# Kernel tuning notes

Measured on AMD Instinct MI355X. Metric: run time of the kernel, lower is better.

## Reference

```python
import jax, jax.numpy as jnp
import numpy as np

H, D, DM, L, B = 16, 64, 1024, 256, 64
SCALE = 1.0 / np.sqrt(D)   # 1/sqrt(d_head)
CHUNK = 64
LN_EPS = 1e-5


def setup_inputs() -> dict:
    key = jax.random.key(0)
    k0, k1, k2, k3 = jax.random.split(key, 4)
    h = jax.random.normal(k0, (L, B, DM), jnp.float32)
    qkv_w = jax.random.normal(k1, (H * 4 * D, DM), jnp.float32) * 0.02
    o_w = jax.random.normal(k2, (DM, H * D), jnp.float32) * 0.02
    ln_gamma = jnp.ones((DM,), jnp.float32)
    ln_beta = jnp.zeros((DM,), jnp.float32)
    pi0 = jax.random.uniform(k3, (H, 256), jnp.float32)
    return {"h": h, "qkv_w": qkv_w, "o_w": o_w,
            "ln_gamma": ln_gamma, "ln_beta": ln_beta, "pi0": pi0}


def _phi(x):
    # elu(x) + 1, then sum-normalize over feature dim
    e = jax.nn.elu(x) + 1.0
    return e / e.sum(-1, keepdims=True)


def _fast_weight_sum(q, k, v):
    # q,k,v: [B,H,L,D]. out[t] = q_t @ W_t, W_t = sum_{s<=t} k_s v_s^T (inclusive).
    # Chunked-recurrent form: intra-chunk causal GEMM + inter-chunk carried state.
    Bb, Hh, Ll, Dd = q.shape
    nc = Ll // CHUNK
    rs = lambda x: x.reshape(Bb, Hh, nc, CHUNK, Dd).transpose(2, 0, 1, 3, 4)  # [nc,B,H,C,D]
    qc, kc, vc = rs(q), rs(k), rs(v)
    mask = jnp.tril(jnp.ones((CHUNK, CHUNK), q.dtype))  # inclusive causal

    def step(W, xs):
        qi, ki, vi = xs  # [B,H,C,D]
        scores = jnp.einsum('bhtd,bhsd->bhts', qi, ki) * mask
        out = jnp.einsum('bhts,bhsd->bhtd', scores, vi) \
            + jnp.einsum('bhtd,bhde->bhte', qi, W)
        W = W + jnp.einsum('bhsd,bhse->bhde', ki, vi)
        return W, out

    W0 = jnp.zeros((Bb, Hh, Dd, Dd), q.dtype)
    _, outs = jax.lax.scan(step, W0, (qc, kc, vc))  # outs: [nc,B,H,C,D]
    return outs.transpose(1, 2, 0, 3, 4).reshape(Bb, Hh, Ll, Dd)


def reference(h, qkv_w, o_w, ln_gamma, ln_beta, pi0):
    slen, bsz, _ = h.shape
    # qkv projection and head split (rbf2keys: q, k1, k2, v)
    qkv = (h @ qkv_w.T).reshape(slen, bsz, H, 4 * D)
    hq, hk1, hk2, hv = jnp.split(qkv, 4, axis=-1)       # each [L,B,H,D]
    perm = lambda x: x.transpose(1, 2, 0, 3)            # -> [B,H,L,D]
    hq, hk1, hk2, hv = perm(hq), perm(hk1), perm(hk2), perm(hv)

    hq = _phi(hq)
    hk1 = _phi(hk1)
    hk2 = _phi(hk2)

    out1 = _fast_weight_sum(hq, hk1, hv)
    out2 = _fast_weight_sum(hq, hk2, hv)

    # skip_attn_normalization=True path: pi0-gated mixture of the two memories
    p = jnp.clip(pi0, 0.0, 1.0)[None, :, :slen, None]   # [1,H,L,1]
    layer_out = SCALE * (out1 * p + out2 * (1.0 - p))   # [B,H,L,D]

    # [B,H,L,D] -> [L,B,H*D]
    layer_out = layer_out.transpose(0, 2, 1, 3).reshape(bsz, slen, H * D).transpose(1, 0, 2)
    attn_out = layer_out @ o_w.T                        # [L,B,DM]

    # post-LN residual (pre_lnorm=False)
    x = h + attn_out
    mu = x.mean(-1, keepdims=True)
    var = ((x - mu) ** 2).mean(-1, keepdims=True)
    return (x - mu) / jnp.sqrt(var + LN_EPS) * ln_gamma + ln_beta
```

## Files before the change

kernel.cpp:

```cpp
#include <hip/hip_runtime.h>
#include <type_traits>


typedef short v8s __attribute__((ext_vector_type(8)));
typedef float v4f __attribute__((ext_vector_type(4)));

__device__ __forceinline__ float bf2f(short s) {
    unsigned int u = ((unsigned int)(unsigned short)s) << 16;
    float f;
    __builtin_memcpy(&f, &u, 4);
    return f;
}
__device__ __forceinline__ short f2bf(float f) {
    unsigned int u;
    __builtin_memcpy(&u, &f, 4);
    u = u + 0x7fffu + ((u >> 16) & 1u);
    return (short)(u >> 16);
}

__device__ __forceinline__ void load_lds16(const short* g, short* l) {
    __builtin_amdgcn_global_load_lds((const __attribute__((address_space(1))) void*)g,
                                     (__attribute__((address_space(3))) void*)l, 16, 0, 0);
}

__global__ void __launch_bounds__(256)
cvt_bf16(const float* __restrict__ in, short* __restrict__ out, int n4) {
    int i = blockIdx.x * 256 + threadIdx.x;
    if (i >= n4) return;
    float4 v = ((const float4*)in)[i];
    short4 o;
    o.x = f2bf(v.x); o.y = f2bf(v.y); o.z = f2bf(v.z); o.w = f2bf(v.w);
    ((short4*)out)[i] = o;
}

template <typename OutT>
__global__ void __launch_bounds__(512, 2)
gemm_nt(const short* __restrict__ Ap, const short* __restrict__ Bp,
        OutT* __restrict__ C, int M, int N, int K) {
    __shared__ __align__(16) short lds[2][2][256 * 64];

    const int tid = threadIdx.x;
    const int w = tid >> 6, lane = tid & 63;
    const int wm = w >> 2, wn = w & 3;
    const int lq = lane >> 4, lr = lane & 15;
    const int asw = (lr & 7) * 8;
    const int rr = tid >> 3;
    const int scol = ((tid & 7) * 8) ^ ((rr & 7) * 8);

    int bid = blockIdx.y * gridDim.x + blockIdx.x;
    int bm, bn;
    if (gridDim.x == 64) {
        int xcd = bid & 7, u = bid >> 3;
        bm = xcd * 8 + (u & 7);
        bn = u >> 3;
    } else {
        int nwg = gridDim.x * gridDim.y;
        int swz = (bid & 7) * (nwg >> 3) + (bid >> 3);
        bm = swz % gridDim.x; bn = swz / gridDim.x;
    }

    v4f acc[8][4] = {};
    v8s a[4][2];
    v8s b[2][2][2];

    const int NT = K >> 6;
    const int nIter = NT >> 1;

#define BAR_() do { asm volatile("" ::: "memory"); __builtin_amdgcn_s_barrier(); asm volatile("" ::: "memory"); } while (0)
#define SBAR_() __builtin_amdgcn_sched_barrier(0)
#define VMCNT4_() asm volatile("s_waitcnt vmcnt(4)" ::: "memory")
#define STAGE_(MAT, BUF, HALF, KT) do { \
        const short* g_ = ((MAT) ? Bp : Ap) + \
            (long)(((MAT) ? bn : bm) * 256 + (HALF) * 128 + rr) * K + (KT) * 64 + scol; \
        short* l_ = &lds[BUF][MAT][(HALF) * 8192] + w * 512; \
        load_lds16(g_, l_); \
        load_lds16(g_ + (long)64 * K, l_ + 4096); \
    } while (0)
#define LDA_(QM, BUF) do { \
        _Pragma("unroll") \
        for (int mi = 0; mi < 4; ++mi) { \
            const short* pa_ = &lds[BUF][0][(wm * 128 + (QM) * 64 + mi * 16 + lr) * 64]; \
            a[mi][0] = *(const v8s*)&pa_[(lq * 8) ^ asw]; \
            a[mi][1] = *(const v8s*)&pa_[(32 + lq * 8) ^ asw]; \
        } \
    } while (0)
#define LDB_(QN, BUF) do { \
        _Pragma("unroll") \
        for (int ni = 0; ni < 2; ++ni) { \
            const short* pb_ = &lds[BUF][1][(wn * 64 + (QN) * 32 + ni * 16 + lr) * 64]; \
            b[QN][ni][0] = *(const v8s*)&pb_[(lq * 8) ^ asw]; \
            b[QN][ni][1] = *(const v8s*)&pb_[(32 + lq * 8) ^ asw]; \
        } \
    } while (0)
#define MFMA_(QM, QN) do { \
        __builtin_amdgcn_s_setprio(1); \
        _Pragma("unroll") \
        for (int kk = 0; kk < 2; ++kk) \
            _Pragma("unroll") \
            for (int mi = 0; mi < 4; ++mi) \
                _Pragma("unroll") \
                for (int ni = 0; ni < 2; ++ni) \
                    acc[(QM) * 4 + mi][(QN) * 2 + ni] = __builtin_amdgcn_mfma_f32_16x16x32_bf16( \
                        a[mi][kk], b[QN][ni][kk], acc[(QM) * 4 + mi][(QN) * 2 + ni], 0, 0, 0); \
        __builtin_amdgcn_s_setprio(0); \
    } while (0)

    STAGE_(1, 0, 0, 0);
    STAGE_(1, 0, 1, 0);
    STAGE_(0, 0, 0, 0);
    STAGE_(0, 0, 1, 0);
    STAGE_(1, 1, 0, 1);
    STAGE_(1, 1, 1, 1);
    VMCNT4_();
    BAR_();

    for (int it = 0; it < nIter; ++it) {
        const int t1 = 2 * it + 1;
        int t2 = 2 * it + 2; if (t2 >= NT) t2 -= NT;
        int t3 = 2 * it + 3; if (t3 >= NT) t3 -= NT;

        LDA_(0, 0); LDB_(0, 0); LDB_(1, 0);
        STAGE_(0, 1, 0, t1);
        MFMA_(0, 0);
        SBAR_(); BAR_();
        STAGE_(0, 1, 1, t1);
        MFMA_(0, 1);
        SBAR_();
        LDA_(1, 0);
        SBAR_(); BAR_();
        STAGE_(1, 0, 0, t2);
        MFMA_(1, 0);
        SBAR_(); BAR_();
        STAGE_(1, 0, 1, t2);
        VMCNT4_();
        MFMA_(1, 1);
        SBAR_(); BAR_();
        LDA_(0, 1); LDB_(0, 1); LDB_(1, 1);
        STAGE_(0, 0, 0, t2);
        MFMA_(0, 0);
        SBAR_(); BAR_();
        STAGE_(0, 0, 1, t2);
        MFMA_(0, 1);
        SBAR_();
        LDA_(1, 1);
        SBAR_(); BAR_();
        STAGE_(1, 1, 0, t3);
        MFMA_(1, 0);
        SBAR_(); BAR_();
        STAGE_(1, 1, 1, t3);
        VMCNT4_();
        MFMA_(1, 1);
        SBAR_(); BAR_();
    }

#undef BAR_
#undef SBAR_
#undef VMCNT4_
#undef STAGE_
#undef LDA_
#undef LDB_
#undef MFMA_

#pragma unroll
    for (int m = 0; m < 8; ++m)
#pragma unroll
        for (int n = 0; n < 4; ++n)
#pragma unroll
            for (int r = 0; r < 4; ++r) {
                int row = bm * 256 + wm * 128 + m * 16 + lq * 4 + r;
                int col = bn * 256 + wn * 64 + n * 16 + lr;
                float v = acc[m][n][r];
                if constexpr (std::is_same_v<OutT, short>)
                    C[(long)row * N + col] = f2bf(v);
                else
                    C[(long)row * N + col] = v;
            }
}

#define SZF(row, col) (((row) << 6) + ((col) ^ (((row) & 7) << 3)))
#define LGKM0_() do { asm volatile("s_waitcnt lgkmcnt(0)" ::: "memory"); __builtin_amdgcn_sched_barrier(0); } while (0)

__device__ __forceinline__ void phi_lane(short* area, int lane) {
    v8s r[8];
#pragma unroll
    for (int g = 0; g < 8; g++)
        r[g] = *(const v8s*)&area[SZF(lane, g * 8)];
    float s = 0.f;
#pragma unroll
    for (int g = 0; g < 8; g++)
#pragma unroll
        for (int k = 0; k < 8; k++) {
            float x = bf2f(r[g][k]);
            s += x > 0.f ? x + 1.f : __expf(x);
        }
    float inv = 1.f / s;
#pragma unroll
    for (int g = 0; g < 8; g++) {
        v8s o;
#pragma unroll
        for (int k = 0; k < 8; k++) {
            float x = bf2f(r[g][k]);
            float e = x > 0.f ? x + 1.f : __expf(x);
            o[k] = f2bf(e * inv);
        }
        *(v8s*)&area[SZF(lane, g * 8)] = o;
    }
}

__device__ __forceinline__ void transpose_lane(short* area, int lane) {
    v8s r[8];
#pragma unroll
    for (int g = 0; g < 8; g++)
        r[g] = *(const v8s*)&area[SZF(lane, g * 8)];
    LGKM0_();
#pragma unroll
    for (int g = 0; g < 8; g++)
#pragma unroll
        for (int k = 0; k < 8; k++)
            area[SZF(g * 8 + k, lane)] = r[g][k];
}

__global__ void __launch_bounds__(64)
fwA(const short* __restrict__ qkv, short* __restrict__ wpre) {
    const int bid = blockIdx.x;
    const int b = bid & 63, h = (bid >> 6) & 15, mem = bid >> 10;
    const int lane = threadIdx.x;
    const int lq = lane >> 4, lr = lane & 15;
    __shared__ __align__(16) short Ak[4096];
    __shared__ __align__(16) short Av[4096];

    const int srow = lane >> 3;
    const int scolw = ((lane & 7) ^ (srow & 7)) << 3;
    const int koff = 64 + mem * 64;

    v4f wacc[4][4] = {};

    for (int c = 0; c < 3; c++) {
        LGKM0_();
        {
            const short* g = qkv + ((long)((c * 64 + srow) * 64 + b)) * 4096 + h * 256 + koff + scolw;
#pragma unroll
            for (int i = 0; i < 8; i++)
                load_lds16(g + (long)i * 8 * 64 * 4096, Ak + i * 512);
        }
        {
            const short* g = qkv + ((long)((c * 64 + srow) * 64 + b)) * 4096 + h * 256 + 192 + scolw;
#pragma unroll
            for (int i = 0; i < 8; i++)
                load_lds16(g + (long)i * 8 * 64 * 4096, Av + i * 512);
        }
        asm volatile("s_waitcnt vmcnt(0)" ::: "memory");
        __builtin_amdgcn_sched_barrier(0);

        phi_lane(Ak, lane);
        transpose_lane(Av, lane);
        LGKM0_();

        v8s vf[4][2];
#pragma unroll
        for (int i = 0; i < 4; i++)
#pragma unroll
            for (int kk = 0; kk < 2; kk++)
                vf[i][kk] = *(const v8s*)&Av[SZF(16 * i + lr, 32 * kk + 8 * lq)];
#pragma unroll
        for (int n = 0; n < 4; n++) {
            v8s ktb[2];
#pragma unroll
            for (int kk = 0; kk < 2; kk++) {
                v8s t;
#pragma unroll
                for (int e = 0; e < 8; e++)
                    t[e] = Ak[SZF(32 * kk + 8 * lq + e, 16 * n + lr)];
                ktb[kk] = t;
            }
#pragma unroll
            for (int i = 0; i < 4; i++) {
                wacc[i][n] = __builtin_amdgcn_mfma_f32_16x16x32_bf16(vf[i][0], ktb[0], wacc[i][n], 0, 0, 0);
                wacc[i][n] = __builtin_amdgcn_mfma_f32_16x16x32_bf16(vf[i][1], ktb[1], wacc[i][n], 0, 0, 0);
            }
        }
        short* wp = wpre + (((long)(mem * 3 + c) * 16 + h) * 64 + b) * 4096;
#pragma unroll
        for (int i = 0; i < 4; i++)
#pragma unroll
            for (int n = 0; n < 4; n++)
#pragma unroll
                for (int r2 = 0; r2 < 4; r2++)
                    wp[(16 * i + lq * 4 + r2) * 64 + 16 * n + lr] = f2bf(wacc[i][n][r2]);
    }
}

__global__ void __launch_bounds__(256)
fwB(const short* __restrict__ qkv, const short* __restrict__ wpre,
    const float* __restrict__ pi0, short* __restrict__ outm) {
    const int bid = blockIdx.x;
    const int b = bid & 63, h = (bid >> 6) & 15, c = bid >> 10;
    const int tid = threadIdx.x;
    const int wv = tid >> 6, lane = tid & 63;
    const int lq = lane >> 4, lr = lane & 15;
    __shared__ __align__(16) short sq[4096];
    __shared__ __align__(16) short sk1[4096];
    __shared__ __align__(16) short sk2[4096];
    __shared__ __align__(16) short svT[4096];

    const int srow = lane >> 3;
    const int scolw = ((lane & 7) ^ (srow & 7)) << 3;

    {
        short* area = (wv == 0) ? sq : (wv == 1) ? sk1 : (wv == 2) ? sk2 : svT;
        const short* g = qkv + ((long)((c * 64 + srow) * 64 + b)) * 4096 + h * 256 + wv * 64 + scolw;
#pragma unroll
        for (int i = 0; i < 8; i++)
            load_lds16(g + (long)i * 8 * 64 * 4096, area + i * 512);
    }
    asm volatile("s_waitcnt vmcnt(0)" ::: "memory");
    __syncthreads();

    if (wv == 0)      phi_lane(sq, lane);
    else if (wv == 1) phi_lane(sk1, lane);
    else if (wv == 2) phi_lane(sk2, lane);
    else              transpose_lane(svT, lane);
    __syncthreads();

    v8s qa[2];
    qa[0] = *(const v8s*)&sq[SZF(16 * wv + lr, 8 * lq)];
    qa[1] = *(const v8s*)&sq[SZF(16 * wv + lr, 32 + 8 * lq)];

    v8s wb1[4][2], wb2[4][2];
    if (c > 0) {
        const short* w1 = wpre + (((long)(0 * 3 + (c - 1)) * 16 + h) * 64 + b) * 4096;
        const short* w2 = wpre + (((long)(1 * 3 + (c - 1)) * 16 + h) * 64 + b) * 4096;
#pragma unroll
        for (int n = 0; n < 4; n++)
#pragma unroll
            for (int kk = 0; kk < 2; kk++) {
                wb1[n][kk] = *(const v8s*)&w1[(16 * n + lr) * 64 + 32 * kk + 8 * lq];
                wb2[n][kk] = *(const v8s*)&w2[(16 * n + lr) * 64 + 32 * kk + 8 * lq];
            }
    }
    float pv[4];
#pragma unroll
    for (int r2 = 0; r2 < 4; r2++) {
        float p = pi0[h * 256 + c * 64 + 16 * wv + lq * 4 + r2];
        pv[r2] = fminf(fmaxf(p, 0.f), 1.f);
    }

    v4f sacc1[4], sacc2[4];
#pragma unroll
    for (int n = 0; n < 4; n++) {
        v8s b10 = *(const v8s*)&sk1[SZF(16 * n + lr, 8 * lq)];
        v8s b11 = *(const v8s*)&sk1[SZF(16 * n + lr, 32 + 8 * lq)];
        v8s b20 = *(const v8s*)&sk2[SZF(16 * n + lr, 8 * lq)];
        v8s b21 = *(const v8s*)&sk2[SZF(16 * n + lr, 32 + 8 * lq)];
        v4f t1 = {}, t2 = {};
        t1 = __builtin_amdgcn_mfma_f32_16x16x32_bf16(qa[0], b10, t1, 0, 0, 0);
        t2 = __builtin_amdgcn_mfma_f32_16x16x32_bf16(qa[0], b20, t2, 0, 0, 0);
        t1 = __builtin_amdgcn_mfma_f32_16x16x32_bf16(qa[1], b11, t1, 0, 0, 0);
        t2 = __builtin_amdgcn_mfma_f32_16x16x32_bf16(qa[1], b21, t2, 0, 0, 0);
        sacc1[n] = t1; sacc2[n] = t2;
    }
    __syncthreads();

#pragma unroll
    for (int n = 0; n < 4; n++)
#pragma unroll
        for (int r2 = 0; r2 < 4; r2++) {
            int t_ = 16 * wv + lq * 4 + r2;
            int s_ = 16 * n + lr;
            sk1[SZF(t_, s_)] = f2bf(s_ <= t_ ? sacc1[n][r2] : 0.f);
            sk2[SZF(t_, s_)] = f2bf(s_ <= t_ ? sacc2[n][r2] : 0.f);
        }
    LGKM0_();

    v8s sa1[2], sa2[2];
    sa1[0] = *(const v8s*)&sk1[SZF(16 * wv + lr, 8 * lq)];
    sa1[1] = *(const v8s*)&sk1[SZF(16 * wv + lr, 32 + 8 * lq)];
    sa2[0] = *(const v8s*)&sk2[SZF(16 * wv + lr, 8 * lq)];
    sa2[1] = *(const v8s*)&sk2[SZF(16 * wv + lr, 32 + 8 * lq)];

#pragma unroll
    for (int j = 0; j < 4; j++) {
        v8s vb0 = *(const v8s*)&svT[SZF(16 * j + lr, 8 * lq)];
        v8s vb1 = *(const v8s*)&svT[SZF(16 * j + lr, 32 + 8 * lq)];
        v4f t1 = {}, t2 = {};
        t1 = __builtin_amdgcn_mfma_f32_16x16x32_bf16(sa1[0], vb0, t1, 0, 0, 0);
        t2 = __builtin_amdgcn_mfma_f32_16x16x32_bf16(sa2[0], vb0, t2, 0, 0, 0);
        t1 = __builtin_amdgcn_mfma_f32_16x16x32_bf16(sa1[1], vb1, t1, 0, 0, 0);
        t2 = __builtin_amdgcn_mfma_f32_16x16x32_bf16(sa2[1], vb1, t2, 0, 0, 0);
        if (c > 0) {
            t1 = __builtin_amdgcn_mfma_f32_16x16x32_bf16(qa[0], wb1[j][0], t1, 0, 0, 0);
            t2 = __builtin_amdgcn_mfma_f32_16x16x32_bf16(qa[0], wb2[j][0], t2, 0, 0, 0);
            t1 = __builtin_amdgcn_mfma_f32_16x16x32_bf16(qa[1], wb1[j][1], t1, 0, 0, 0);
            t2 = __builtin_amdgcn_mfma_f32_16x16x32_bf16(qa[1], wb2[j][1], t2, 0, 0, 0);
        }
#pragma unroll
        for (int r2 = 0; r2 < 4; r2++) {
            int t_ = 16 * wv + lq * 4 + r2;
            float val = 0.125f * (pv[r2] * t1[r2] + (1.f - pv[r2]) * t2[r2]);
            outm[((long)((c * 64 + t_) * 64 + b)) * 1024 + h * 64 + 16 * j + lr] = f2bf(val);
        }
    }
}

__global__ void __launch_bounds__(256)
ln_kernel(const float* __restrict__ h, const float* __restrict__ attn,
          const float* __restrict__ gamma, const float* __restrict__ beta,
          float* __restrict__ out) {
    const int row = blockIdx.x;
    const long base = (long)row * 1024;
    const int tid = threadIdx.x;
    float4 xh = ((const float4*)(h + base))[tid];
    float4 xa = ((const float4*)(attn + base))[tid];
    float4 x;
    x.x = xh.x + xa.x; x.y = xh.y + xa.y; x.z = xh.z + xa.z; x.w = xh.w + xa.w;
    float s = x.x + x.y + x.z + x.w;
    float s2 = x.x * x.x + x.y * x.y + x.z * x.z + x.w * x.w;
#pragma unroll
    for (int m = 32; m > 0; m >>= 1) {
        s += __shfl_xor(s, m, 64);
        s2 += __shfl_xor(s2, m, 64);
    }
    __shared__ float ps[4], ps2[4];
    int w = tid >> 6, lane = tid & 63;
    if (lane == 0) { ps[w] = s; ps2[w] = s2; }
    __syncthreads();
    s = ps[0] + ps[1] + ps[2] + ps[3];
    s2 = ps2[0] + ps2[1] + ps2[2] + ps2[3];
    float mu = s * (1.f / 1024.f);
    float var = s2 * (1.f / 1024.f) - mu * mu;
    float inv = rsqrtf(var + 1e-5f);
    float4 g = ((const float4*)gamma)[tid];
    float4 bb = ((const float4*)beta)[tid];
    float4 o;
    o.x = (x.x - mu) * inv * g.x + bb.x;
    o.y = (x.y - mu) * inv * g.y + bb.y;
    o.z = (x.z - mu) * inv * g.z + bb.z;
    o.w = (x.w - mu) * inv * g.w + bb.w;
    ((float4*)(out + base))[tid] = o;
}

extern "C" void kernel_launch(void* const* d_in, const int* in_sizes, int n_in,
                              void* d_out, int out_size, void* d_ws, size_t ws_size,
                              hipStream_t stream) {
    const float* h     = (const float*)d_in[0];
    const float* qkvw  = (const float*)d_in[1];
    const float* ow    = (const float*)d_in[2];
    const float* gamma = (const float*)d_in[3];
    const float* beta  = (const float*)d_in[4];
    const float* pi0   = (const float*)d_in[5];
    float* out = (float*)d_out;
    char* ws = (char*)d_ws;

    short* h_bf   = (short*)(ws);
    short* wq_bf  = (short*)(ws + 33554432);
    short* wo_bf  = (short*)(ws + 41943040);
    short* qkv_bf = (short*)(ws + 44040192);
    short* wpre   = (short*)(ws + 178257920);
    float* attnf  = (float*)(ws + 44040192);
    short* lmix   = h_bf;

    cvt_bf16<<<16384, 256, 0, stream>>>(h, h_bf, 16777216 / 4);
    cvt_bf16<<<4096, 256, 0, stream>>>(qkvw, wq_bf, 4194304 / 4);
    cvt_bf16<<<1024, 256, 0, stream>>>(ow, wo_bf, 1048576 / 4);

    gemm_nt<short><<<dim3(64, 16), 512, 0, stream>>>(h_bf, wq_bf, qkv_bf, 16384, 4096, 1024);

    fwA<<<2048, 64, 0, stream>>>(qkv_bf, wpre);
    fwB<<<4096, 256, 0, stream>>>(qkv_bf, wpre, pi0, lmix);

    gemm_nt<float><<<dim3(64, 4), 512, 0, stream>>>(lmix, wo_bf, attnf, 16384, 1024, 1024);

    ln_kernel<<<16384, 256, 0, stream>>>(h, attnf, gamma, beta, out);
}
```

Measured before the change: 412.0 us.

## Shrink GEMM tiles to 256x128xK32, stage fwA stores and fwB weights via LDS

The GEMM is retiled from 256x256 with K-step 64 to 256x128 with K-step 32. This cuts LDS per block so four blocks can share a CU, and doubles the grid. The swizzle and pipeline schedule are rewritten to match, with a single B load per stage. Separately, fwA now stages its fast-weight output through LDS so it can write coalesced 16-byte rows, and fwB loads the carried state into LDS asynchronously instead of doing strided global reads. The smaller tiles lower per-block arithmetic intensity and add more barriers per unit of work, while fwB grows its shared-memory footprint.

```diff
diff --git a/kernel.cpp b/kernel.cpp
--- a/kernel.cpp
+++ b/kernel.cpp
@@ -34,84 +34,68 @@
 }
 
 template <typename OutT>
-__global__ void __launch_bounds__(512, 2)
+__global__ void __launch_bounds__(512, 4)
 gemm_nt(const short* __restrict__ Ap, const short* __restrict__ Bp,
         OutT* __restrict__ C, int M, int N, int K) {
-    __shared__ __align__(16) short lds[2][2][256 * 64];
+    __shared__ __align__(16) short ldsA[2][256 * 32];
+    __shared__ __align__(16) short ldsB[2][128 * 32];
 
     const int tid = threadIdx.x;
     const int w = tid >> 6, lane = tid & 63;
     const int wm = w >> 2, wn = w & 3;
     const int lq = lane >> 4, lr = lane & 15;
-    const int asw = (lr & 7) * 8;
-    const int rr = tid >> 3;
-    const int scol = ((tid & 7) * 8) ^ ((rr & 7) * 8);
+    const int asw = (lq ^ ((lr >> 1) & 3)) * 8;
+    const int rr = tid >> 2;
+    const int scol = ((tid & 3) ^ ((rr >> 1) & 3)) * 8;
 
     int bid = blockIdx.y * gridDim.x + blockIdx.x;
-    int bm, bn;
-    if (gridDim.x == 64) {
-        int xcd = bid & 7, u = bid >> 3;
-        bm = xcd * 8 + (u & 7);
-        bn = u >> 3;
-    } else {
-        int nwg = gridDim.x * gridDim.y;
-        int swz = (bid & 7) * (nwg >> 3) + (bid >> 3);
-        bm = swz % gridDim.x; bn = swz / gridDim.x;
-    }
-
-    v4f acc[8][4] = {};
-    v8s a[4][2];
-    v8s b[2][2][2];
-
-    const int NT = K >> 6;
+    int xcd = bid & 7, u = bid >> 3;
+    int bm = xcd * 8 + (u & 7);
+    int bn = u >> 3;
+
+    v4f acc[8][2] = {};
+    v8s a[4], b[2];
+
+    const int NT = K >> 5;
     const int nIter = NT >> 1;
+
+    const short* baseA0 = Ap + (long)(bm * 256 + rr) * K + scol;
+    const short* baseA1 = baseA0 + (long)128 * K;
+    const short* baseB  = Bp + (long)(bn * 128 + rr) * K + scol;
 
 #define BAR_() do { asm volatile("" ::: "memory"); __builtin_amdgcn_s_barrier(); asm volatile("" ::: "memory"); } while (0)
 #define SBAR_() __builtin_amdgcn_sched_barrier(0)
-#define VMCNT4_() asm volatile("s_waitcnt vmcnt(4)" ::: "memory")
-#define STAGE_(MAT, BUF, HALF, KT) do { \
-        const short* g_ = ((MAT) ? Bp : Ap) + \
-            (long)(((MAT) ? bn : bm) * 256 + (HALF) * 128 + rr) * K + (KT) * 64 + scol; \
-        short* l_ = &lds[BUF][MAT][(HALF) * 8192] + w * 512; \
-        load_lds16(g_, l_); \
-        load_lds16(g_ + (long)64 * K, l_ + 4096); \
+#define VMCNT1_() asm volatile("s_waitcnt vmcnt(1)" ::: "memory")
+#define STAGEA_(BUF, HALF, KT) \
+    load_lds16(((HALF) ? baseA1 : baseA0) + (KT) * 32, &ldsA[BUF][(HALF) * 4096 + w * 512])
+#define STAGEB_(BUF, KT) \
+    load_lds16(baseB + (KT) * 32, &ldsB[BUF][w * 512])
+#define LDA_(H, BUF) do { \
+        _Pragma("unroll") \
+        for (int mi = 0; mi < 4; ++mi) \
+            a[mi] = *(const v8s*)&ldsA[BUF][(wm * 128 + (H) * 64 + mi * 16 + lr) * 32 + asw]; \
     } while (0)
-#define LDA_(QM, BUF) do { \
+#define LDB_(BUF) do { \
         _Pragma("unroll") \
-        for (int mi = 0; mi < 4; ++mi) { \
-            const short* pa_ = &lds[BUF][0][(wm * 128 + (QM) * 64 + mi * 16 + lr) * 64]; \
-            a[mi][0] = *(const v8s*)&pa_[(lq * 8) ^ asw]; \
-            a[mi][1] = *(const v8s*)&pa_[(32 + lq * 8) ^ asw]; \
-        } \
+        for (int ni = 0; ni < 2; ++ni) \
+            b[ni] = *(const v8s*)&ldsB[BUF][(wn * 32 + ni * 16 + lr) * 32 + asw]; \
     } while (0)
-#define LDB_(QN, BUF) do { \
-        _Pragma("unroll") \
-        for (int ni = 0; ni < 2; ++ni) { \
-            const short* pb_ = &lds[BUF][1][(wn * 64 + (QN) * 32 + ni * 16 + lr) * 64]; \
-            b[QN][ni][0] = *(const v8s*)&pb_[(lq * 8) ^ asw]; \
-            b[QN][ni][1] = *(const v8s*)&pb_[(32 + lq * 8) ^ asw]; \
-        } \
-    } while (0)
-#define MFMA_(QM, QN) do { \
+#define MFMA_(H) do { \
         __builtin_amdgcn_s_setprio(1); \
         _Pragma("unroll") \
-        for (int kk = 0; kk < 2; ++kk) \
+        for (int mi = 0; mi < 4; ++mi) \
             _Pragma("unroll") \
-            for (int mi = 0; mi < 4; ++mi) \
-                _Pragma("unroll") \
-                for (int ni = 0; ni < 2; ++ni) \
-                    acc[(QM) * 4 + mi][(QN) * 2 + ni] = __builtin_amdgcn_mfma_f32_16x16x32_bf16( \
-                        a[mi][kk], b[QN][ni][kk], acc[(QM) * 4 + mi][(QN) * 2 + ni], 0, 0, 0); \
+            for (int ni = 0; ni < 2; ++ni) \
+                acc[(H) * 4 + mi][ni] = __builtin_amdgcn_mfma_f32_16x16x32_bf16( \
+                    a[mi], b[ni], acc[(H) * 4 + mi][ni], 0, 0, 0); \
         __builtin_amdgcn_s_setprio(0); \
     } while (0)
 
-    STAGE_(1, 0, 0, 0);
-    STAGE_(1, 0, 1, 0);
-    STAGE_(0, 0, 0, 0);
-    STAGE_(0, 0, 1, 0);
-    STAGE_(1, 1, 0, 1);
-    STAGE_(1, 1, 1, 1);
-    VMCNT4_();
+    STAGEB_(0, 0);
+    STAGEA_(0, 0, 0);
+    STAGEA_(0, 1, 0);
+    STAGEB_(1, 1);
+    VMCNT1_();
     BAR_();
 
     for (int it = 0; it < nIter; ++it) {
@@ -119,44 +103,37 @@
         int t2 = 2 * it + 2; if (t2 >= NT) t2 -= NT;
         int t3 = 2 * it + 3; if (t3 >= NT) t3 -= NT;
 
-        LDA_(0, 0); LDB_(0, 0); LDB_(1, 0);
-        STAGE_(0, 1, 0, t1);
-        MFMA_(0, 0);
-        SBAR_(); BAR_();
-        STAGE_(0, 1, 1, t1);
-        MFMA_(0, 1);
+        LDA_(0, 0); LDB_(0);
+        STAGEA_(1, 0, t1);
+        MFMA_(0);
         SBAR_();
         LDA_(1, 0);
         SBAR_(); BAR_();
-        STAGE_(1, 0, 0, t2);
-        MFMA_(1, 0);
-        SBAR_(); BAR_();
-        STAGE_(1, 0, 1, t2);
-        VMCNT4_();
-        MFMA_(1, 1);
-        SBAR_(); BAR_();
-        LDA_(0, 1); LDB_(0, 1); LDB_(1, 1);
-        STAGE_(0, 0, 0, t2);
-        MFMA_(0, 0);
-        SBAR_(); BAR_();
-        STAGE_(0, 0, 1, t2);
-        MFMA_(0, 1);
+        STAGEA_(1, 1, t1);
+        STAGEB_(0, t2);
+        MFMA_(1);
+        SBAR_();
+        VMCNT1_();
+        BAR_();
+        LDA_(0, 1); LDB_(1);
+        STAGEA_(0, 0, t2);
+        MFMA_(0);
         SBAR_();
         LDA_(1, 1);
         SBAR_(); BAR_();
-        STAGE_(1, 1, 0, t3);
-        MFMA_(1, 0);
-        SBAR_(); BAR_();
-        STAGE_(1, 1, 1, t3);
-        VMCNT4_();
-        MFMA_(1, 1);
-        SBAR_(); BAR_();
+        STAGEA_(0, 1, t2);
+        STAGEB_(1, t3);
+        MFMA_(1);
+        SBAR_();
+        VMCNT1_();
+        BAR_();
     }
 
 #undef BAR_
 #undef SBAR_
-#undef VMCNT4_
-#undef STAGE_
+#undef VMCNT1_
+#undef STAGEA_
+#undef STAGEB_
 #undef LDA_
 #undef LDB_
 #undef MFMA_
@@ -164,11 +141,11 @@
 #pragma unroll
     for (int m = 0; m < 8; ++m)
 #pragma unroll
-        for (int n = 0; n < 4; ++n)
+        for (int n = 0; n < 2; ++n)
 #pragma unroll
             for (int r = 0; r < 4; ++r) {
                 int row = bm * 256 + wm * 128 + m * 16 + lq * 4 + r;
-                int col = bn * 256 + wn * 64 + n * 16 + lr;
+                int col = bn * 128 + wn * 32 + n * 16 + lr;
                 float v = acc[m][n][r];
                 if constexpr (std::is_same_v<OutT, short>)
                     C[(long)row * N + col] = f2bf(v);
@@ -279,14 +256,21 @@
                 wacc[i][n] = __builtin_amdgcn_mfma_f32_16x16x32_bf16(vf[i][1], ktb[1], wacc[i][n], 0, 0, 0);
             }
         }
+        LGKM0_();
+#pragma unroll
+        for (int i = 0; i < 4; i++)
+#pragma unroll
+            for (int n = 0; n < 4; n++)
+#pragma unroll
+                for (int r2 = 0; r2 < 4; r2++)
+                    Av[SZF(16 * i + lq * 4 + r2, 16 * n + lr)] = f2bf(wacc[i][n][r2]);
+        LGKM0_();
         short* wp = wpre + (((long)(mem * 3 + c) * 16 + h) * 64 + b) * 4096;
 #pragma unroll
-        for (int i = 0; i < 4; i++)
-#pragma unroll
-            for (int n = 0; n < 4; n++)
-#pragma unroll
-                for (int r2 = 0; r2 < 4; r2++)
-                    wp[(16 * i + lq * 4 + r2) * 64 + 16 * n + lr] = f2bf(wacc[i][n][r2]);
+        for (int g = 0; g < 8; g++) {
+            v8s t = *(const v8s*)&Av[SZF(lane, g * 8)];
+            *(v8s*)(wp + lane * 64 + g * 8) = t;
+        }
     }
 }
 
@@ -302,6 +286,8 @@
     __shared__ __align__(16) short sk1[4096];
     __shared__ __align__(16) short sk2[4096];
     __shared__ __align__(16) short svT[4096];
+    __shared__ __align__(16) short sw1[4096];
+    __shared__ __align__(16) short sw2[4096];
 
     const int srow = lane >> 3;
     const int scolw = ((lane & 7) ^ (srow & 7)) << 3;
@@ -312,6 +298,14 @@
 #pragma unroll
         for (int i = 0; i < 8; i++)
             load_lds16(g + (long)i * 8 * 64 * 4096, area + i * 512);
+    }
+    if (c > 0 && wv < 2) {
+        short* area = wv ? sw2 : sw1;
+        const short* g = wpre + (((long)(wv * 3 + (c - 1)) * 16 + h) * 64 + b) * 4096
+                       + srow * 64 + scolw;
+#pragma unroll
+        for (int i = 0; i < 8; i++)
+            load_lds16(g + (long)i * 8 * 64, area + i * 512);
     }
     asm volatile("s_waitcnt vmcnt(0)" ::: "memory");
     __syncthreads();
@@ -328,14 +322,12 @@
 
     v8s wb1[4][2], wb2[4][2];
     if (c > 0) {
-        const short* w1 = wpre + (((long)(0 * 3 + (c - 1)) * 16 + h) * 64 + b) * 4096;
-        const short* w2 = wpre + (((long)(1 * 3 + (c - 1)) * 16 + h) * 64 + b) * 4096;
 #pragma unroll
         for (int n = 0; n < 4; n++)
 #pragma unroll
             for (int kk = 0; kk < 2; kk++) {
-                wb1[n][kk] = *(const v8s*)&w1[(16 * n + lr) * 64 + 32 * kk + 8 * lq];
-                wb2[n][kk] = *(const v8s*)&w2[(16 * n + lr) * 64 + 32 * kk + 8 * lq];
+                wb1[n][kk] = *(const v8s*)&sw1[SZF(16 * n + lr, 32 * kk + 8 * lq)];
+                wb2[n][kk] = *(const v8s*)&sw2[SZF(16 * n + lr, 32 * kk + 8 * lq)];
             }
     }
     float pv[4];
@@ -463,12 +455,12 @@
     cvt_bf16<<<4096, 256, 0, stream>>>(qkvw, wq_bf, 4194304 / 4);
     cvt_bf16<<<1024, 256, 0, stream>>>(ow, wo_bf, 1048576 / 4);
 
-    gemm_nt<short><<<dim3(64, 16), 512, 0, stream>>>(h_bf, wq_bf, qkv_bf, 16384, 4096, 1024);
+    gemm_nt<short><<<dim3(64, 32), 512, 0, stream>>>(h_bf, wq_bf, qkv_bf, 16384, 4096, 1024);
 
     fwA<<<2048, 64, 0, stream>>>(qkv_bf, wpre);
     fwB<<<4096, 256, 0, stream>>>(qkv_bf, wpre, pi0, lmix);
 
-    gemm_nt<float><<<dim3(64, 4), 512, 0, stream>>>(lmix, wo_bf, attnf, 16384, 1024, 1024);
+    gemm_nt<float><<<dim3(64, 8), 512, 0, stream>>>(lmix, wo_bf, attnf, 16384, 1024, 1024);
 
     ln_kernel<<<16384, 256, 0, stream>>>(h, attnf, gamma, beta, out);
 }
```

New measurement: 429.4 us. +4.2%, slower.
